# Kernel optimization log

Measured on AMD Instinct MI355X. Metric: run time of the kernel, lower is better.

Reference implementation:

```python
import jax, jax.numpy as jnp
import numpy as np

B, S, D, H = 2, 4096, 512, 8
DH = D // H
EPS = 1e-5


def setup_inputs() -> dict:
    key = jax.random.key(0)
    ks = jax.random.split(key, 8)
    s = 0.02
    return {
        "x": jax.random.normal(ks[0], (B, S, D), jnp.float32),
        "in_proj_w": jax.random.normal(ks[1], (3 * D, D), jnp.float32) * s,
        "in_proj_b": jnp.zeros((3 * D,), jnp.float32),
        "out_proj_w": jax.random.normal(ks[2], (D, D), jnp.float32) * s,
        "out_proj_b": jnp.zeros((D,), jnp.float32),
        "ln1_g": jnp.ones((D,), jnp.float32),
        "ln1_b": jnp.zeros((D,), jnp.float32),
        "ln2_g": jnp.ones((D,), jnp.float32),
        "ln2_b": jnp.zeros((D,), jnp.float32),
        "w1": jax.random.normal(ks[3], (D, D), jnp.float32) * s,
        "b1": jnp.zeros((D,), jnp.float32),
        "w2": jax.random.normal(ks[4], (D, D), jnp.float32) * s,
        "b2": jnp.zeros((D,), jnp.float32),
        "window": 256,
    }


def _layernorm(x, g, b):
    mu = jnp.mean(x, axis=-1, keepdims=True)
    var = jnp.mean(jnp.square(x - mu), axis=-1, keepdims=True)
    return (x - mu) * jax.lax.rsqrt(var + EPS) * g + b


def reference(x, in_proj_w, in_proj_b, out_proj_w, out_proj_b,
              ln1_g, ln1_b, ln2_g, ln2_b, w1, b1, w2, b2, window):
    b, s, d = x.shape
    # sliding-window mask: allowed iff |i - j| <= window
    idx = jnp.arange(s)
    allowed = jnp.abs(idx[:, None] - idx[None, :]) <= window  # [S,S]

    # fused QKV projection (torch MultiheadAttention layout: W [3D, D])
    qkv = x @ in_proj_w.T + in_proj_b  # [B,S,3D]
    q, k, v = jnp.split(qkv, 3, axis=-1)
    q = q.reshape(b, s, H, DH)
    k = k.reshape(b, s, H, DH)
    v = v.reshape(b, s, H, DH)

    scale = 1.0 / jnp.sqrt(jnp.float32(DH))
    scores = jnp.einsum("bqhd,bkhd->bhqk", q, k) * scale  # [B,H,S,S]
    scores = jnp.where(allowed[None, None], scores, -jnp.inf)
    attn = jax.nn.softmax(scores, axis=-1)
    ctx = jnp.einsum("bhqk,bkhd->bqhd", attn, v).reshape(b, s, d)
    attn_out = ctx @ out_proj_w.T + out_proj_b

    # residual + LayerNorm (dropout rate 0 -> identity)
    h = _layernorm(x + attn_out, ln1_g, ln1_b)
    mlp = jax.nn.relu(h @ w1.T + b1) @ w2.T + b2
    return _layernorm(h + mlp, ln2_g, ln2_b)
```

## Files before the change

kernel.cpp:

```cpp
#include <hip/hip_runtime.h>

typedef __bf16 bf16;
typedef __bf16 bf16x2 __attribute__((ext_vector_type(2)));
typedef __bf16 bf16x8 __attribute__((ext_vector_type(8)));
typedef float f32x4 __attribute__((ext_vector_type(4)));

#define S_LEN 4096
#define DMODEL 512
#define NHEAD 8
#define DHEAD 64
#define BATCH 2
#define M_ROWS (BATCH * S_LEN)
#define K_DIM 512
#define QKV_LD 1536

__device__ __forceinline__ void async16(void* lds, const void* g) {
  __builtin_amdgcn_global_load_lds(
      (const __attribute__((address_space(1))) unsigned int*)g,
      (__attribute__((address_space(3))) unsigned int*)lds, 16, 0, 0);
}

__global__ void detect_dtype(const unsigned int* __restrict__ x,
                             int* __restrict__ flag) {
  const int lane = threadIdx.x;
  int cnt = 0;
#pragma unroll
  for (int i = 0; i < 16; ++i) {
    const unsigned int w = x[lane * 16 + i];
    const unsigned int e = (w >> 7) & 0xFFu;
    cnt += (e >= 100u && e <= 140u) ? 1 : 0;
  }
#pragma unroll
  for (int off = 1; off < 64; off <<= 1) cnt += __shfl_xor(cnt, off);
  if (lane == 0) *flag = (cnt >= 700) ? 1 : 0;
}

__device__ __forceinline__ bf16x8 ld8(const void* p, size_t e, bool asF32) {
  if (asF32) {
    const float* q = (const float*)p + e;
    const float4 a = *(const float4*)q;
    const float4 b = *(const float4*)(q + 4);
    bf16x8 r;
    r[0] = (bf16)a.x; r[1] = (bf16)a.y; r[2] = (bf16)a.z; r[3] = (bf16)a.w;
    r[4] = (bf16)b.x; r[5] = (bf16)b.y; r[6] = (bf16)b.z; r[7] = (bf16)b.w;
    return r;
  }
  return *(const bf16x8*)((const bf16*)p + e);
}

__device__ __forceinline__ float ld1(const void* p, size_t e, bool asF32) {
  return asF32 ? ((const float*)p)[e] : (float)((const bf16*)p)[e];
}

__global__ __launch_bounds__(256) void cvt_all(const void* __restrict__ x,
                                               const void* __restrict__ s0,
                                               const void* __restrict__ s1,
                                               const void* __restrict__ s2,
                                               const void* __restrict__ s3,
                                               bf16* __restrict__ xb,
                                               bf16* __restrict__ warena,
                                               const int* __restrict__ flag) {
  const bool f32in = (*flag == 0);
  const int b = blockIdx.x;
  if (b < 2048) {
    const size_t idx = ((size_t)b * 256 + threadIdx.x) * 8;
    *(bf16x8*)(xb + idx) = ld8(x, idx, f32in);
    return;
  }
  const int wb = b - 2048;
  const void* s;
  size_t doff;
  int lb;
  if (wb < 384)      { s = s0; doff = 0;        lb = wb; }
  else if (wb < 512) { s = s1; doff = 786432;   lb = wb - 384; }
  else if (wb < 640) { s = s2; doff = 1048576;  lb = wb - 512; }
  else               { s = s3; doff = 1310720;  lb = wb - 640; }
  const size_t idx = (size_t)lb * 2048 + threadIdx.x * 8;
  *(bf16x8*)(warena + doff + idx) = ld8(s, idx, f32in);
}

template <int NMAT, int BN, bool RELU>
__global__ __launch_bounds__(256) void gemm_bt(const bf16* __restrict__ A,
                                               const bf16* __restrict__ W,
                                               const void* __restrict__ bias,
                                               bf16* __restrict__ C,
                                               const int* __restrict__ flag) {
  __shared__ __align__(16) bf16 As[128 * 64];
  __shared__ __align__(16) bf16 Ws[BN * 64];

  const bool f32in = (*flag == 0);

  const int t = threadIdx.x;
  const int lane = t & 63;
  const int wave = t >> 6;
  constexpr int MT = (BN == 128) ? 4 : 2;
  const int wm = (BN == 128) ? (wave >> 1) * 64 : wave * 32;
  const int wn = (BN == 128) ? (wave & 1) * 64 : 0;
  const int l16 = lane & 15;
  const int quad = lane >> 4;

  constexpr int NB = NMAT / BN;
  constexpr int MPX = (M_ROWS / 128) / 8;
  const int bid = blockIdx.x;
  const int xcd = bid & 7;
  const int r = bid >> 3;
  const int m0 = (xcd * MPX + r / NB) * 128;
  const int n0 = (r % NB) * BN;

  const int rr = lane >> 3;
  const int cb = (lane & 7) ^ rr;
  const int sw = l16 & 7;

  f32x4 acc[MT][4];
#pragma unroll
  for (int i = 0; i < MT; ++i)
#pragma unroll
    for (int j = 0; j < 4; ++j) acc[i][j] = (f32x4){0.f, 0.f, 0.f, 0.f};

  for (int kt = 0; kt < K_DIM; kt += 64) {
    __syncthreads();
#pragma unroll
    for (int i = 0; i < 4; ++i) {
      const int r0 = wave * 32 + i * 8;
      async16(&As[r0 * 64], &A[(size_t)(m0 + r0 + rr) * K_DIM + kt + cb * 8]);
    }
#pragma unroll
    for (int i = 0; i < BN / 32; ++i) {
      const int r0 = wave * (BN / 4) + i * 8;
      async16(&Ws[r0 * 64], &W[(size_t)(n0 + r0 + rr) * K_DIM + kt + cb * 8]);
    }
    __syncthreads();
#pragma unroll
    for (int ks = 0; ks < 2; ++ks) {
      bf16x8 af[MT], wf[4];
#pragma unroll
      for (int mt = 0; mt < MT; ++mt)
        af[mt] = *(const bf16x8*)&As[(wm + mt * 16 + l16) * 64 +
                                     (((ks * 4 + quad) ^ sw) * 8)];
#pragma unroll
      for (int nt = 0; nt < 4; ++nt)
        wf[nt] = *(const bf16x8*)&Ws[(wn + nt * 16 + l16) * 64 +
                                     (((ks * 4 + quad) ^ sw) * 8)];
#pragma unroll
      for (int mt = 0; mt < MT; ++mt)
#pragma unroll
        for (int nt = 0; nt < 4; ++nt)
          acc[mt][nt] = __builtin_amdgcn_mfma_f32_16x16x32_bf16(af[mt], wf[nt],
                                                                acc[mt][nt], 0, 0, 0);
    }
  }

#pragma unroll
  for (int nt = 0; nt < 4; ++nt) {
    const int n = n0 + wn + nt * 16 + l16;
    const float bv = ld1(bias, n, f32in);
#pragma unroll
    for (int mt = 0; mt < MT; ++mt) {
#pragma unroll
      for (int r4 = 0; r4 < 4; ++r4) {
        const int m = m0 + wm + mt * 16 + quad * 4 + r4;
        float v = acc[mt][nt][r4] + bv;
        if (RELU) v = fmaxf(v, 0.f);
        C[(size_t)m * NMAT + n] = (bf16)v;
      }
    }
  }
}

__global__ __launch_bounds__(256) void attn_fwd(const bf16* __restrict__ qkv,
                                                bf16* __restrict__ ctx,
                                                const int* __restrict__ wptr) {
  __shared__ __align__(16) bf16 Kt[2][64 * 64];
  __shared__ __align__(16) bf16 Vt[2][64][72];
  __shared__ __align__(16) bf16 Pbuf[4][16][72];

  const int t = threadIdx.x;
  const int lane = t & 63;
  const int wave = t >> 6;
  const int l16 = lane & 15;
  const int quad = lane >> 4;
  const int rr = lane >> 3;
  const int cb = (lane & 7) ^ rr;
  const int sw = l16 & 7;

  const int bid = blockIdx.x;
  const int xcd = bid & 7;
  const int jj = bid >> 3;
  const int pair = xcd * 2 + (jj >> 6);
  const int qblk = jj & 63;
  const int h = pair & 7;
  const int b = pair >> 3;
  const int qbase = qblk * 64;
  int window = *wptr;
  if (window < 0) window = 0;
  if (window > S_LEN) window = S_LEN;
  const float sc_log2e = 0.125f * 1.44269504f;

  const int qrow = qbase + wave * 16 + l16;
  const bf16* qp = qkv + (size_t)(b * S_LEN + qrow) * QKV_LD + h * DHEAD;
  const bf16x8 qf0 = *(const bf16x8*)(qp + quad * 8);
  const bf16x8 qf1 = *(const bf16x8*)(qp + 32 + quad * 8);

  f32x4 o[4];
#pragma unroll
  for (int nt = 0; nt < 4; ++nt) o[nt] = (f32x4){0.f, 0.f, 0.f, 0.f};
  float lp[4] = {0.f, 0.f, 0.f, 0.f};

  int kstart = qbase - window;
  if (kstart < 0) kstart = 0;
  kstart &= ~63;
  int kend = qbase + 64 + window;
  if (kend > S_LEN) kend = S_LEN;
  const int niter = (kend - kstart + 63) >> 6;

  const int vk = (t & 31) * 2;
  const int vd = (t >> 5) * 8;
  const bf16* vbase = qkv + (size_t)(b * S_LEN) * QKV_LD + 2 * DMODEL + h * DHEAD + vd;
  const bf16* kbase = qkv + (size_t)(b * S_LEN) * QKV_LD + DMODEL + h * DHEAD;

#pragma unroll
  for (int i = 0; i < 2; ++i) {
    const int r0 = wave * 16 + i * 8;
    async16(&Kt[0][r0 * 64],
            &kbase[(size_t)(kstart + r0 + rr) * QKV_LD + cb * 8]);
  }
  {
    const bf16* p = vbase + (size_t)(kstart + vk) * QKV_LD;
    const bf16x8 va = *(const bf16x8*)p;
    const bf16x8 vb = *(const bf16x8*)(p + QKV_LD);
#pragma unroll
    for (int j = 0; j < 8; ++j) {
      bf16x2 pr; pr[0] = va[j]; pr[1] = vb[j];
      *(bf16x2*)&Vt[0][vd + j][vk] = pr;
    }
  }

  for (int it = 0; it < niter; ++it) {
    const int kt = kstart + it * 64;
    const int cur = it & 1;
    __syncthreads();

    bf16x8 na, nb;
    const bool have_next = (it + 1 < niter);
    if (have_next) {
#pragma unroll
      for (int i = 0; i < 2; ++i) {
        const int r0 = wave * 16 + i * 8;
        async16(&Kt[cur ^ 1][r0 * 64],
                &kbase[(size_t)(kt + 64 + r0 + rr) * QKV_LD + cb * 8]);
      }
      const bf16* p = vbase + (size_t)(kt + 64 + vk) * QKV_LD;
      na = *(const bf16x8*)p;
      nb = *(const bf16x8*)(p + QKV_LD);
    }

    f32x4 s[4];
#pragma unroll
    for (int t4 = 0; t4 < 4; ++t4) s[t4] = (f32x4){0.f, 0.f, 0.f, 0.f};
#pragma unroll
    for (int t4 = 0; t4 < 4; ++t4) {
      const int row = t4 * 16 + l16;
      const bf16x8 k0 = *(const bf16x8*)&Kt[cur][row * 64 + ((quad ^ sw) * 8)];
      const bf16x8 k1 =
          *(const bf16x8*)&Kt[cur][row * 64 + (((4 + quad) ^ sw) * 8)];
      s[t4] = __builtin_amdgcn_mfma_f32_16x16x32_bf16(qf0, k0, s[t4], 0, 0, 0);
      s[t4] = __builtin_amdgcn_mfma_f32_16x16x32_bf16(qf1, k1, s[t4], 0, 0, 0);
    }

#pragma unroll
    for (int r = 0; r < 4; ++r) {
      const int q = qbase + wave * 16 + quad * 4 + r;
      const int lo = q - window, hi = q + window;
      float psum = 0.f;
#pragma unroll
      for (int t4 = 0; t4 < 4; ++t4) {
        const int key = kt + t4 * 16 + l16;
        const float p = (key >= lo && key <= hi)
                            ? __builtin_amdgcn_exp2f(s[t4][r] * sc_log2e)
                            : 0.f;
        psum += p;
        Pbuf[wave][quad * 4 + r][t4 * 16 + l16] = (bf16)p;
      }
      lp[r] += psum;
    }

    const bf16x8 pf0 = *(const bf16x8*)&Pbuf[wave][l16][quad * 8];
    const bf16x8 pf1 = *(const bf16x8*)&Pbuf[wave][l16][32 + quad * 8];
#pragma unroll
    for (int nt = 0; nt < 4; ++nt) {
      const bf16x8 v0 = *(const bf16x8*)&Vt[cur][nt * 16 + l16][quad * 8];
      const bf16x8 v1 = *(const bf16x8*)&Vt[cur][nt * 16 + l16][32 + quad * 8];
      o[nt] = __builtin_amdgcn_mfma_f32_16x16x32_bf16(pf0, v0, o[nt], 0, 0, 0);
      o[nt] = __builtin_amdgcn_mfma_f32_16x16x32_bf16(pf1, v1, o[nt], 0, 0, 0);
    }

    if (have_next) {
#pragma unroll
      for (int j = 0; j < 8; ++j) {
        bf16x2 pr; pr[0] = na[j]; pr[1] = nb[j];
        *(bf16x2*)&Vt[cur ^ 1][vd + j][vk] = pr;
      }
    }
  }

#pragma unroll
  for (int r = 0; r < 4; ++r) {
#pragma unroll
    for (int off = 1; off < 16; off <<= 1) lp[r] += __shfl_xor(lp[r], off);
    const float inv = (lp[r] > 0.f) ? (1.0f / lp[r]) : 0.f;
    const int q = qbase + wave * 16 + quad * 4 + r;
#pragma unroll
    for (int nt = 0; nt < 4; ++nt) {
      ctx[(size_t)(b * S_LEN + q) * DMODEL + h * DHEAD + nt * 16 + l16] =
          (bf16)(o[nt][r] * inv);
    }
  }
}

template <bool A_RAW, bool OUT_RAW>
__global__ __launch_bounds__(256) void ln_fused(const void* __restrict__ a,
                                                const bf16* __restrict__ bres,
                                                const void* __restrict__ g,
                                                const void* __restrict__ be,
                                                void* __restrict__ out,
                                                const int* __restrict__ flag) {
  const bool f32in = (*flag == 0);
  const int row = blockIdx.x * 4 + (threadIdx.x >> 6);
  const int lane = threadIdx.x & 63;
  const size_t base = (size_t)row * DMODEL + lane * 8;
  const bf16x8 va = ld8(a, base, A_RAW && f32in);
  const bf16x8 vb = *(const bf16x8*)(bres + base);
  float v[8], s = 0.f, s2 = 0.f;
#pragma unroll
  for (int j = 0; j < 8; ++j) {
    v[j] = (float)va[j] + (float)vb[j];
    s += v[j];
    s2 += v[j] * v[j];
  }
#pragma unroll
  for (int off = 1; off < 64; off <<= 1) {
    s += __shfl_xor(s, off);
    s2 += __shfl_xor(s2, off);
  }
  const float mean = s * (1.0f / DMODEL);
  float var = s2 * (1.0f / DMODEL) - mean * mean;
  if (var < 0.f) var = 0.f;
  const float rstd = rsqrtf(var + 1e-5f);
  const bf16x8 gv = ld8(g, lane * 8, f32in);
  const bf16x8 bev = ld8(be, lane * 8, f32in);
  float ov[8];
#pragma unroll
  for (int j = 0; j < 8; ++j)
    ov[j] = (v[j] - mean) * rstd * (float)gv[j] + (float)bev[j];
  if (OUT_RAW && f32in) {
    float4 o0 = {ov[0], ov[1], ov[2], ov[3]};
    float4 o1 = {ov[4], ov[5], ov[6], ov[7]};
    *(float4*)((float*)out + base) = o0;
    *(float4*)((float*)out + base + 4) = o1;
  } else {
    bf16x8 ob;
#pragma unroll
    for (int j = 0; j < 8; ++j) ob[j] = (bf16)ov[j];
    *(bf16x8*)((bf16*)out + base) = ob;
  }
}

extern "C" void kernel_launch(void* const* d_in, const int* in_sizes, int n_in,
                              void* d_out, int out_size, void* d_ws, size_t ws_size,
                              hipStream_t stream) {
  const void* x          = d_in[0];
  const void* in_proj_w  = d_in[1];
  const void* in_proj_b  = d_in[2];
  const void* out_proj_w = d_in[3];
  const void* out_proj_b = d_in[4];
  const void* ln1_g      = d_in[5];
  const void* ln1_b      = d_in[6];
  const void* ln2_g      = d_in[7];
  const void* ln2_b      = d_in[8];
  const void* w1         = d_in[9];
  const void* b1         = d_in[10];
  const void* w2         = d_in[11];
  const void* b2         = d_in[12];
  const int*  wptr       = (const int*)d_in[13];

  char* ws = (char*)d_ws;
  int* flag = (int*)ws;
  bf16* warena = (bf16*)(ws + 256);
  bf16* wq = warena;
  bf16* wo = warena + 786432;
  bf16* w1b = warena + 1048576;
  bf16* w2b = warena + 1310720;
  char* big = ws + 256 + 3145728;
  bf16* qkv      = (bf16*)big;
  bf16* h        = (bf16*)big;
  bf16* a1       = (bf16*)(big + 8388608);
  bf16* attn_out = (bf16*)(big + 16777216);
  bf16* mlp      = attn_out;
  bf16* xb       = (bf16*)d_out;
  bf16* ctx      = (bf16*)d_out;

  detect_dtype<<<1, 64, 0, stream>>>((const unsigned int*)x, flag);
  cvt_all<<<2816, 256, 0, stream>>>(x, in_proj_w, out_proj_w, w1, w2, xb, warena, flag);
  gemm_bt<QKV_LD, 128, false><<<768, 256, 0, stream>>>(
      xb, wq, in_proj_b, qkv, flag);
  attn_fwd<<<dim3(BATCH * NHEAD * (S_LEN / 64)), 256, 0, stream>>>(qkv, ctx, wptr);
  gemm_bt<DMODEL, 64, false><<<512, 256, 0, stream>>>(
      ctx, wo, out_proj_b, attn_out, flag);
  ln_fused<true, false><<<dim3(M_ROWS / 4), 256, 0, stream>>>(
      x, attn_out, ln1_g, ln1_b, h, flag);
  gemm_bt<DMODEL, 64, true><<<512, 256, 0, stream>>>(
      h, w1b, b1, a1, flag);
  gemm_bt<DMODEL, 64, false><<<512, 256, 0, stream>>>(
      a1, w2b, b2, mlp, flag);
  ln_fused<false, true><<<dim3(M_ROWS / 4), 256, 0, stream>>>(
      h, mlp, ln2_g, ln2_b, d_out, flag);
}
```

Baseline: 205.5 us.

## Double-buffer GEMM LDS tiles and fold dtype detection into conversion kernel

```diff
diff --git a/kernel.cpp b/kernel.cpp
--- a/kernel.cpp
+++ b/kernel.cpp
@@ -20,9 +20,7 @@
       (__attribute__((address_space(3))) unsigned int*)lds, 16, 0, 0);
 }
 
-__global__ void detect_dtype(const unsigned int* __restrict__ x,
-                             int* __restrict__ flag) {
-  const int lane = threadIdx.x;
+__device__ __forceinline__ int detect_bf16(const unsigned int* x, int lane) {
   int cnt = 0;
 #pragma unroll
   for (int i = 0; i < 16; ++i) {
@@ -32,7 +30,7 @@
   }
 #pragma unroll
   for (int off = 1; off < 64; off <<= 1) cnt += __shfl_xor(cnt, off);
-  if (lane == 0) *flag = (cnt >= 700) ? 1 : 0;
+  return (cnt >= 700) ? 1 : 0;
 }
 
 __device__ __forceinline__ bf16x8 ld8(const void* p, size_t e, bool asF32) {
@@ -59,9 +57,11 @@
                                                const void* __restrict__ s3,
                                                bf16* __restrict__ xb,
                                                bf16* __restrict__ warena,
-                                               const int* __restrict__ flag) {
-  const bool f32in = (*flag == 0);
+                                               int* __restrict__ flag) {
+  const int isbf = detect_bf16((const unsigned int*)x, threadIdx.x & 63);
+  const bool f32in = (isbf == 0);
   const int b = blockIdx.x;
+  if (b == 0 && threadIdx.x == 0) *flag = isbf;
   if (b < 2048) {
     const size_t idx = ((size_t)b * 256 + threadIdx.x) * 8;
     *(bf16x8*)(xb + idx) = ld8(x, idx, f32in);
@@ -85,8 +85,8 @@
                                                const void* __restrict__ bias,
                                                bf16* __restrict__ C,
                                                const int* __restrict__ flag) {
-  __shared__ __align__(16) bf16 As[128 * 64];
-  __shared__ __align__(16) bf16 Ws[BN * 64];
+  __shared__ __align__(16) bf16 As[2][128 * 64];
+  __shared__ __align__(16) bf16 Ws[2][BN * 64];
 
   const bool f32in = (*flag == 0);
 
@@ -117,30 +117,38 @@
 #pragma unroll
     for (int j = 0; j < 4; ++j) acc[i][j] = (f32x4){0.f, 0.f, 0.f, 0.f};
 
-  for (int kt = 0; kt < K_DIM; kt += 64) {
-    __syncthreads();
+  auto stage = [&](int buf, int kt) {
 #pragma unroll
     for (int i = 0; i < 4; ++i) {
       const int r0 = wave * 32 + i * 8;
-      async16(&As[r0 * 64], &A[(size_t)(m0 + r0 + rr) * K_DIM + kt + cb * 8]);
+      async16(&As[buf][r0 * 64],
+              &A[(size_t)(m0 + r0 + rr) * K_DIM + kt + cb * 8]);
     }
 #pragma unroll
     for (int i = 0; i < BN / 32; ++i) {
       const int r0 = wave * (BN / 4) + i * 8;
-      async16(&Ws[r0 * 64], &W[(size_t)(n0 + r0 + rr) * K_DIM + kt + cb * 8]);
-    }
+      async16(&Ws[buf][r0 * 64],
+              &W[(size_t)(n0 + r0 + rr) * K_DIM + kt + cb * 8]);
+    }
+  };
+
+  stage(0, 0);
+  constexpr int NIT = K_DIM / 64;
+  for (int it = 0; it < NIT; ++it) {
+    const int cur = it & 1;
     __syncthreads();
+    if (it + 1 < NIT) stage(cur ^ 1, (it + 1) * 64);
 #pragma unroll
     for (int ks = 0; ks < 2; ++ks) {
       bf16x8 af[MT], wf[4];
 #pragma unroll
       for (int mt = 0; mt < MT; ++mt)
-        af[mt] = *(const bf16x8*)&As[(wm + mt * 16 + l16) * 64 +
-                                     (((ks * 4 + quad) ^ sw) * 8)];
+        af[mt] = *(const bf16x8*)&As[cur][(wm + mt * 16 + l16) * 64 +
+                                          (((ks * 4 + quad) ^ sw) * 8)];
 #pragma unroll
       for (int nt = 0; nt < 4; ++nt)
-        wf[nt] = *(const bf16x8*)&Ws[(wn + nt * 16 + l16) * 64 +
-                                     (((ks * 4 + quad) ^ sw) * 8)];
+        wf[nt] = *(const bf16x8*)&Ws[cur][(wn + nt * 16 + l16) * 64 +
+                                          (((ks * 4 + quad) ^ sw) * 8)];
 #pragma unroll
       for (int mt = 0; mt < MT; ++mt)
 #pragma unroll
@@ -399,7 +407,6 @@
   bf16* xb       = (bf16*)d_out;
   bf16* ctx      = (bf16*)d_out;
 
-  detect_dtype<<<1, 64, 0, stream>>>((const unsigned int*)x, flag);
   cvt_all<<<2816, 256, 0, stream>>>(x, in_proj_w, out_proj_w, w1, w2, xb, warena, flag);
   gemm_bt<QKV_LD, 128, false><<<768, 256, 0, stream>>>(
       xb, wq, in_proj_b, qkv, flag);
```

New measurement: 207.8 us. About the same (+1.1%).
